# Kernel tuning notes

Measured on AMD Instinct MI355X. Metric: run time of the kernel, lower is better.

The kernel has to match this reference:

```python
import jax, jax.numpy as jnp
import numpy as np
from jax import lax

VOCAB = 256
H = 1024
L = 2
B = 64
T = 512
RESIDUAL = True


def setup_inputs() -> dict:
    key = jax.random.key(0)
    ks = jax.random.split(key, 8)
    s_ih = 1.0 / np.sqrt(H)
    return {
        "X": jax.random.randint(ks[0], (B, T), 0, VOCAB),
        "embed": jax.random.normal(ks[1], (VOCAB, H), dtype=jnp.float32) * 0.02,
        "Wih": jax.random.normal(ks[2], (L, 4 * H, H), dtype=jnp.float32) * s_ih,
        "Whh": jax.random.normal(ks[3], (L, 4 * H, H), dtype=jnp.float32) * s_ih,
        "bih": jax.random.normal(ks[4], (L, 4 * H), dtype=jnp.float32) * s_ih,
        "bhh": jax.random.normal(ks[5], (L, 4 * H), dtype=jnp.float32) * s_ih,
        "Wout": jax.random.normal(ks[6], (VOCAB, H), dtype=jnp.float32) * s_ih,
        "bout": jax.random.normal(ks[7], (VOCAB,), dtype=jnp.float32) * s_ih,
    }


def reference(X, embed, Wih, Whh, bih, bhh, Wout, bout):
    # X: [B, T] int tokens. Original loops over t in [0, T-2]: feeds X[:, t]
    # through an L-layer (residual) LSTM one char at a time, accumulates
    # mean-over-batch cross entropy vs X[:, t+1], then divides by T.
    Bsz, Tlen = X.shape
    n_layers = Wih.shape[0]
    xs = embed[X[:, :-1]]          # [B, T-1, H] embedded inputs
    xs_t = jnp.swapaxes(xs, 0, 1)  # [T-1, B, H] time-major for scan

    def cell(carry, x_t):
        h, c = carry  # each [L, B, H]
        inp = x_t
        hs, cs = [], []
        for l in range(n_layers):
            # torch LSTM gate order: input, forget, cell(g), output
            gates = inp @ Wih[l].T + h[l] @ Whh[l].T + (bih[l] + bhh[l])
            i_g, f_g, g_g, o_g = jnp.split(gates, 4, axis=-1)
            c_l = jax.nn.sigmoid(f_g) * c[l] + jax.nn.sigmoid(i_g) * jnp.tanh(g_g)
            h_l = jax.nn.sigmoid(o_g) * jnp.tanh(c_l)
            hs.append(h_l)
            cs.append(c_l)
            inp = h_l + inp if RESIDUAL else h_l
        return (jnp.stack(hs), jnp.stack(cs)), inp

    init = (jnp.zeros((n_layers, Bsz, xs.shape[-1]), xs.dtype),
            jnp.zeros((n_layers, Bsz, xs.shape[-1]), xs.dtype))
    _, outs = lax.scan(cell, init, xs_t)       # [T-1, B, H]

    logits = outs @ Wout.T + bout              # [T-1, B, V]
    targets = X[:, 1:].T                        # [T-1, B]
    logp = jax.nn.log_softmax(logits, axis=-1)
    ce = -jnp.take_along_axis(logp, targets[..., None], axis=-1)[..., 0]  # [T-1, B]
    loss = ce.mean(axis=1).sum() / Tlen
    return loss
```

## Files before the change

### kernel.cpp

```cpp
#include <hip/hip_runtime.h>
#include <hip/hip_bf16.h>

typedef __hip_bfloat16 bf16;
typedef short v8s __attribute__((ext_vector_type(8)));
typedef float v4f __attribute__((ext_vector_type(4)));
typedef float v16f __attribute__((ext_vector_type(16)));
typedef unsigned long long u64;

static __device__ __forceinline__ float bf2f(bf16 x) { return __bfloat162float(x); }
static __device__ __forceinline__ unsigned short bfbits(float f) {
    bf16 t = __float2bfloat16(f);
    return *(unsigned short*)&t;
}
static __device__ __forceinline__ float fast_tanh(float x) {
    float e = __expf(-2.f * x);
    return (1.f - e) / (1.f + e);
}

__global__ __launch_bounds__(256) void k_zero(float* __restrict__ zbase, float* __restrict__ loss) {
    int idx = blockIdx.x * 256 + threadIdx.x;
    if (idx < 140288) zbase[idx] = 0.0f;
    if (idx == 0) loss[0] = 0.0f;
}

__global__ __launch_bounds__(256) void k_convert_w(const float* __restrict__ Wih,
                                                   const float* __restrict__ Whh,
                                                   bf16* __restrict__ Wb) {
    int idx = blockIdx.x * 256 + threadIdx.x;
    int k2 = idx & 2047;
    int ln = idx >> 11;
    float v = (k2 < 1024) ? Wih[ln * 1024 + k2] : Whh[ln * 1024 + (k2 - 1024)];
    Wb[idx] = __float2bfloat16(v);
}

__global__ __launch_bounds__(256) void k_convert_small(const float* __restrict__ Wout,
                                                       const float* __restrict__ bih,
                                                       const float* __restrict__ bhh,
                                                       bf16* __restrict__ Wob,
                                                       float* __restrict__ bsum) {
    int idx = blockIdx.x * 256 + threadIdx.x;
    if (idx < 262144) Wob[idx] = __float2bfloat16(Wout[idx]);
    int bidx = idx - 262144;
    if (bidx >= 0 && bidx < 8192) bsum[bidx] = bih[bidx] + bhh[bidx];
}

__global__ __launch_bounds__(256) void k_embed(const int* __restrict__ X,
                                               const float* __restrict__ embed,
                                               bf16* __restrict__ x0) {
    int bi = blockIdx.x;
    int kc = bi & 3;
    int tb = bi >> 2;
    int b  = tb & 63;
    int t  = tb >> 6;
    int k  = kc * 256 + threadIdx.x;
    int tok = X[b * 512 + t];
    x0[(long)tb * 1024 + k] = __float2bfloat16(embed[tok * 1024 + k]);
}

#define GLDI_C(dst, p, o) asm volatile("global_load_dwordx4 %0, %1, off offset:%2"         : "=v"(dst) : "v"(p), "i"(o))
#define GLDI_B(dst, p, o) asm volatile("global_load_dwordx4 %0, %1, off offset:%2 sc0 sc1" : "=v"(dst) : "v"(p), "i"(o))
#define MFMA(acc, a, w) asm volatile("v_mfma_f32_32x32x16_bf16 %0, %1, %2, %0" : "+v"(acc) : "v"(a), "a"(w))
#define VW(n)  asm volatile("s_waitcnt vmcnt(%0)" :: "i"(n))
#define VW0()  asm volatile("s_waitcnt vmcnt(0)")
#define ZACC(a) do { _Pragma("unroll") for (int r_ = 0; r_ < 16; ++r_) a[r_] = 0.f; } while(0)

#define ISSUE(GLD, c, B) do { \
    GLD(B[0], pA0, (c)*128 +  0); GLD(B[1], pA1, (c)*128 +  0); \
    GLD(B[2], pA0, (c)*128 + 32); GLD(B[3], pA1, (c)*128 + 32); \
    GLD(B[4], pA0, (c)*128 + 64); GLD(B[5], pA1, (c)*128 + 64); \
    GLD(B[6], pA0, (c)*128 + 96); GLD(B[7], pA1, (c)*128 + 96); } while(0)

#define CHUNK(c, B) do { _Pragma("unroll") for (int i_ = 0; i_ < 4; ++i_) { \
    MFMA(acc00, B[2*i_],   wa0[(c)*4+i_]); \
    MFMA(acc10, B[2*i_+1], wa0[(c)*4+i_]); \
    MFMA(acc01, B[2*i_],   wa1[(c)*4+i_]); \
    MFMA(acc11, B[2*i_+1], wa1[(c)*4+i_]); } } while(0)

#define PIPE(GLD) do { \
    ISSUE(GLD,0,bufa); ISSUE(GLD,1,bufb); ISSUE(GLD,2,bufc); ISSUE(GLD,3,bufd); \
    VW(24); CHUNK(0,bufa); ISSUE(GLD,4,bufa); \
    VW(24); CHUNK(1,bufb); ISSUE(GLD,5,bufb); \
    VW(24); CHUNK(2,bufc); ISSUE(GLD,6,bufc); \
    VW(24); CHUNK(3,bufd); ISSUE(GLD,7,bufd); \
    VW(24); CHUNK(4,bufa); \
    VW(16); CHUNK(5,bufb); \
    VW(8);  CHUNK(6,bufc); \
    VW(0);  CHUNK(7,bufd); } while(0)

#define WRGP(OP) do { _Pragma("unroll") for (int r_ = 0; r_ < 16; ++r_) { \
    const int grow_ = (r_&3) + ((r_>>2)<<3) + ((l>>5)<<2); \
    gp[q&1][grow_][l&31]          OP acc00[r_]; \
    gp[q&1][grow_][32+(l&31)]     OP acc01[r_]; \
    gp[q&1][32+grow_][l&31]       OP acc10[r_]; \
    gp[q&1][32+grow_][32+(l&31)]  OP acc11[r_]; } } while(0)

__global__ __launch_bounds__(256, 1) void k_lstm(bf16* __restrict__ x0all,
                                                 bf16* __restrict__ x1buf,
                                                 bf16* __restrict__ h0buf,
                                                 bf16* __restrict__ h1buf,
                                                 const bf16* __restrict__ Wb,
                                                 const float* __restrict__ bsum,
                                                 unsigned* bar) {
    __shared__ float gp[2][64][67];
    __shared__ float c_lds[64][17];
    __shared__ float b_lds[64];

    const int g     = blockIdx.x;
    const int layer = g >> 6;
    const int j     = g & 63;
    const int tid   = threadIdx.x;
    const int l     = tid & 63;
    const int q     = tid >> 6;

    unsigned* cnt = bar;

    if (tid < 64) b_lds[tid] = bsum[layer * 4096 + (tid >> 4) * 1024 + (j << 4) + (tid & 15)];
    for (int i = tid; i < 64 * 17; i += 256) ((float*)c_lds)[i] = 0.f;

    const int nl0 = l & 31, nl1 = 32 + (l & 31);
    const long N0 = (long)((nl0 >> 4) * 1024 + (j << 4) + (nl0 & 15));
    const long N1 = (long)((nl1 >> 4) * 1024 + (j << 4) + (nl1 & 15));
    const bf16* wp0 = Wb + (long)layer * 8388608 + N0 * 2048 + q * 512 + ((l >> 5) << 3);
    const bf16* wp1 = Wb + (long)layer * 8388608 + N1 * 2048 + q * 512 + ((l >> 5) << 3);
    v8s wa0[32], wa1[32];
#pragma unroll
    for (int kk = 0; kk < 32; ++kk) {
        wa0[kk] = *(const v8s*)(wp0 + kk * 16);
        asm volatile("" : "+a"(wa0[kk]));
        wa1[kk] = *(const v8s*)(wp1 + kk * 16);
        asm volatile("" : "+a"(wa1[kk]));
    }

    const int ab = tid >> 2;
    const int dq = tid & 3;
    const bool prewave = (layer == 0) && (q < 2);

#pragma unroll 1
    for (int s = 0; s < 512; ++s) {
        const bool act = (layer == 0) ? (s < 511) : (s >= 1);
        const bf16* xop = x0all + (long)s * 65536;
        const bf16* x1p = x1buf + ((s + 1) & 1) * 65536;
        const bf16* h0p = h0buf + ((s + 1) & 1) * 65536;
        const bf16* h1p = h1buf + ((s + 1) & 1) * 65536;
        bf16* hdst  = (layer ? h1buf : h0buf) + (s & 1) * 65536;
        bf16* x1dst = x1buf + (s & 1) * 65536;
        bf16* res1  = x0all + (long)(s - 1) * 65536;

        const bf16* base = (layer == 0) ? ((q < 2) ? xop : h0p)
                                        : ((q < 2) ? x1p : h1p);
        const bf16* pA0 = base + ((q & 1) << 9) + (l & 31) * 1024 + ((l >> 5) << 3);
        const bf16* pA1 = pA0 + 32 * 1024;

        v16f acc00, acc01, acc10, acc11;
        v8s bufa[8], bufb[8], bufc[8], bufd[8];

        if (act && prewave) {
            ZACC(acc00); ZACC(acc01); ZACC(acc10); ZACC(acc11);
            PIPE(GLDI_C);
            WRGP(=);
        }
        if (tid == 0 && s > 0) {
            const unsigned tgt = 128u * (unsigned)s;
            while (__hip_atomic_load(cnt, __ATOMIC_RELAXED, __HIP_MEMORY_SCOPE_AGENT) < tgt) {}
        }
        __syncthreads();
        if (act && !prewave) {
            ZACC(acc00); ZACC(acc01); ZACC(acc10); ZACC(acc11);
            PIPE(GLDI_B);
            if (q < 2) WRGP(=);
        }
        __syncthreads();
        if (act && q >= 2) WRGP(+=);
        __syncthreads();

        if (act) {
            u64 xv;
            if (layer == 0) {
                xv = *(const u64*)(xop + ab * 1024 + (j << 4) + dq * 4);
            } else {
                const bf16* xrp = x1p + ab * 1024 + (j << 4) + dq * 4;
                asm volatile("global_load_dwordx2 %0, %1, off sc0 sc1" : "=v"(xv) : "v"(xrp));
            }
            float hv4[4];
#pragma unroll
            for (int i = 0; i < 4; ++i) {
                const int d = dq * 4 + i;
                const float gi = gp[0][ab][d]      + gp[1][ab][d]      + b_lds[d];
                const float gf = gp[0][ab][16 + d] + gp[1][ab][16 + d] + b_lds[16 + d];
                const float gg = gp[0][ab][32 + d] + gp[1][ab][32 + d] + b_lds[32 + d];
                const float go = gp[0][ab][48 + d] + gp[1][ab][48 + d] + b_lds[48 + d];
                const float si = 1.f / (1.f + __expf(-gi));
                const float sf = 1.f / (1.f + __expf(-gf));
                const float so = 1.f / (1.f + __expf(-go));
                const float tg = fast_tanh(gg);
                const float cn = sf * c_lds[ab][d] + si * tg;
                c_lds[ab][d] = cn;
                hv4[i] = so * fast_tanh(cn);
            }
            if (layer != 0) VW0();
            u64 hv64 = 0, rv64 = 0;
#pragma unroll
            for (int i = 0; i < 4; ++i) {
                const unsigned us = (unsigned)((xv >> (16 * i)) & 0xffffu);
                const float rv = hv4[i] + __uint_as_float(us << 16);
                hv64 |= (u64)bfbits(hv4[i]) << (16 * i);
                rv64 |= (u64)bfbits(rv) << (16 * i);
            }
            const int off = ab * 1024 + (j << 4) + dq * 4;
            bf16* hp = hdst + off;
            asm volatile("global_store_dwordx2 %0, %1, off sc0 sc1" :: "v"(hp), "v"(hv64) : "memory");
            if (layer == 0) {
                bf16* rp = x1dst + off;
                asm volatile("global_store_dwordx2 %0, %1, off sc0 sc1" :: "v"(rp), "v"(rv64) : "memory");
            } else {
                *(u64*)(res1 + off) = rv64;
            }
        }
        VW0();
        __syncthreads();
        if (tid == 0)
            __hip_atomic_fetch_add(cnt, 1u, __ATOMIC_RELAXED, __HIP_MEMORY_SCOPE_AGENT);
    }
}

__global__ __launch_bounds__(256) void k_final(const bf16* __restrict__ outAll,
                                               const bf16* __restrict__ Wob,
                                               const float* __restrict__ bout,
                                               const int* __restrict__ X,
                                               float* __restrict__ loss) {
    const int t    = blockIdx.x;
    const int tid  = threadIdx.x;
    const int lane = tid & 63;
    const int w    = tid >> 6;
    const int col  = lane & 15;
    const int oct  = lane >> 4;
    const bf16* arow = outAll + ((long)t * 64 + (w << 4) + col) * 1024 + (oct << 3);
    v4f acc[16];
#pragma unroll
    for (int nt = 0; nt < 16; ++nt) acc[nt] = (v4f){0.f, 0.f, 0.f, 0.f};
    for (int k0 = 0; k0 < 1024; k0 += 32) {
        v8s a = *(const v8s*)(arow + k0);
#pragma unroll
        for (int nt = 0; nt < 16; ++nt) {
            v8s bb = *(const v8s*)(Wob + ((nt << 4) + col) * 1024 + (oct << 3) + k0);
            acc[nt] = __builtin_amdgcn_mfma_f32_16x16x32_bf16(a, bb, acc[nt], 0, 0, 0);
        }
    }
#pragma unroll
    for (int nt = 0; nt < 16; ++nt) {
        const float bb = bout[(nt << 4) + col];
        acc[nt][0] += bb; acc[nt][1] += bb; acc[nt][2] += bb; acc[nt][3] += bb;
    }
    float ce_sum = 0.f;
#pragma unroll
    for (int r = 0; r < 4; ++r) {
        float mx = -3.4e38f;
#pragma unroll
        for (int nt = 0; nt < 16; ++nt) mx = fmaxf(mx, acc[nt][r]);
#pragma unroll
        for (int mm = 1; mm < 16; mm <<= 1) mx = fmaxf(mx, __shfl_xor(mx, mm, 64));
        float ss = 0.f;
#pragma unroll
        for (int nt = 0; nt < 16; ++nt) ss += __expf(acc[nt][r] - mx);
#pragma unroll
        for (int mm = 1; mm < 16; mm <<= 1) ss += __shfl_xor(ss, mm, 64);
        const int b   = (w << 4) + (oct << 2) + r;
        const int tok = X[b * 512 + t + 1];
        float lt = 0.f;
#pragma unroll
        for (int nt = 0; nt < 16; ++nt)
            if ((tok >> 4) == nt) lt = acc[nt][r];
        if ((tok & 15) == col)
            ce_sum += mx + __logf(ss) - lt;
    }
#pragma unroll
    for (int mm = 1; mm < 64; mm <<= 1) ce_sum += __shfl_xor(ce_sum, mm, 64);
    if (lane == 0) atomicAdd(loss, ce_sum * (1.0f / 32768.0f));
}

extern "C" void kernel_launch(void* const* d_in, const int* in_sizes, int n_in,
                              void* d_out, int out_size, void* d_ws, size_t ws_size,
                              hipStream_t stream) {
    const int*   X     = (const int*)  d_in[0];
    const float* embed = (const float*)d_in[1];
    const float* Wih   = (const float*)d_in[2];
    const float* Whh   = (const float*)d_in[3];
    const float* bih   = (const float*)d_in[4];
    const float* bhh   = (const float*)d_in[5];
    const float* Wout  = (const float*)d_in[6];
    const float* bout  = (const float*)d_in[7];
    float* loss = (float*)d_out;

    char* ws = (char*)d_ws;
    bf16*     x0all = (bf16*)(ws + 0);
    bf16*     Wb    = (bf16*)(ws + 66977792);
    bf16*     Wob   = (bf16*)(ws + 100532224);
    bf16*     x1buf = (bf16*)(ws + 101056512);
    bf16*     h0buf = (bf16*)(ws + 101318656);
    bf16*     h1buf = (bf16*)(ws + 101580800);
    float*    bsum  = (float*)(ws + 101842944);
    unsigned* bar   = (unsigned*)(ws + 101875712);
    float*    zbase = (float*)(ws + 101318656);

    if (ws_size < 101879808u) return;

    k_zero<<<548, 256, 0, stream>>>(zbase, loss);
    k_convert_w<<<65536, 256, 0, stream>>>(Wih, Whh, Wb);
    k_convert_small<<<1056, 256, 0, stream>>>(Wout, bih, bhh, Wob, bsum);
    k_embed<<<130816, 256, 0, stream>>>(X, embed, x0all);

    void* args[] = {&x0all, &x1buf, &h0buf, &h1buf, &Wb, &bsum, &bar};
    hipLaunchCooperativeKernel((void*)k_lstm, dim3(128), dim3(256), args, 0, stream);

    k_final<<<511, 256, 0, stream>>>(x0all, Wob, bout, X, loss);
}
```

Before: 6.822 ms.

## Split grid barrier counter into per-group cache lines with acquire fence

Replaces the single global arrival counter with 16 counters, one per group of 8 blocks, each on its own cache line. Layer-0 blocks wait only on layer-0 lines, and layer-1 blocks wait on all lines. The spin loop takes the minimum over the lines, sleeps briefly between polls, and issues an agent-scope acquire fence. Activation loads now use ordinary cached loads instead of sc0 sc1 system-coherent loads, relying on the fence for visibility. This aims to cut atomic contention and the cost of coherent loads, at the risk of stale data if the fence does not cover non-coherent L2 paths.

Result: no change. 6.742 ms (-1.2%).

```diff
diff --git a/kernel.cpp b/kernel.cpp
--- a/kernel.cpp
+++ b/kernel.cpp
@@ -57,18 +57,17 @@
     x0[(long)tb * 1024 + k] = __float2bfloat16(embed[tok * 1024 + k]);
 }
 
-#define GLDI_C(dst, p, o) asm volatile("global_load_dwordx4 %0, %1, off offset:%2"         : "=v"(dst) : "v"(p), "i"(o))
-#define GLDI_B(dst, p, o) asm volatile("global_load_dwordx4 %0, %1, off offset:%2 sc0 sc1" : "=v"(dst) : "v"(p), "i"(o))
+#define GLDI(dst, p, o) asm volatile("global_load_dwordx4 %0, %1, off offset:%2" : "=v"(dst) : "v"(p), "i"(o))
 #define MFMA(acc, a, w) asm volatile("v_mfma_f32_32x32x16_bf16 %0, %1, %2, %0" : "+v"(acc) : "v"(a), "a"(w))
 #define VW(n)  asm volatile("s_waitcnt vmcnt(%0)" :: "i"(n))
 #define VW0()  asm volatile("s_waitcnt vmcnt(0)")
 #define ZACC(a) do { _Pragma("unroll") for (int r_ = 0; r_ < 16; ++r_) a[r_] = 0.f; } while(0)
 
-#define ISSUE(GLD, c, B) do { \
-    GLD(B[0], pA0, (c)*128 +  0); GLD(B[1], pA1, (c)*128 +  0); \
-    GLD(B[2], pA0, (c)*128 + 32); GLD(B[3], pA1, (c)*128 + 32); \
-    GLD(B[4], pA0, (c)*128 + 64); GLD(B[5], pA1, (c)*128 + 64); \
-    GLD(B[6], pA0, (c)*128 + 96); GLD(B[7], pA1, (c)*128 + 96); } while(0)
+#define ISSUE(c, B) do { \
+    GLDI(B[0], pA0, (c)*128 +  0); GLDI(B[1], pA1, (c)*128 +  0); \
+    GLDI(B[2], pA0, (c)*128 + 32); GLDI(B[3], pA1, (c)*128 + 32); \
+    GLDI(B[4], pA0, (c)*128 + 64); GLDI(B[5], pA1, (c)*128 + 64); \
+    GLDI(B[6], pA0, (c)*128 + 96); GLDI(B[7], pA1, (c)*128 + 96); } while(0)
 
 #define CHUNK(c, B) do { _Pragma("unroll") for (int i_ = 0; i_ < 4; ++i_) { \
     MFMA(acc00, B[2*i_],   wa0[(c)*4+i_]); \
@@ -76,12 +75,12 @@
     MFMA(acc01, B[2*i_],   wa1[(c)*4+i_]); \
     MFMA(acc11, B[2*i_+1], wa1[(c)*4+i_]); } } while(0)
 
-#define PIPE(GLD) do { \
-    ISSUE(GLD,0,bufa); ISSUE(GLD,1,bufb); ISSUE(GLD,2,bufc); ISSUE(GLD,3,bufd); \
-    VW(24); CHUNK(0,bufa); ISSUE(GLD,4,bufa); \
-    VW(24); CHUNK(1,bufb); ISSUE(GLD,5,bufb); \
-    VW(24); CHUNK(2,bufc); ISSUE(GLD,6,bufc); \
-    VW(24); CHUNK(3,bufd); ISSUE(GLD,7,bufd); \
+#define PIPE() do { \
+    ISSUE(0,bufa); ISSUE(1,bufb); ISSUE(2,bufc); ISSUE(3,bufd); \
+    VW(24); CHUNK(0,bufa); ISSUE(4,bufa); \
+    VW(24); CHUNK(1,bufb); ISSUE(5,bufb); \
+    VW(24); CHUNK(2,bufc); ISSUE(6,bufc); \
+    VW(24); CHUNK(3,bufd); ISSUE(7,bufd); \
     VW(24); CHUNK(4,bufa); \
     VW(16); CHUNK(5,bufb); \
     VW(8);  CHUNK(6,bufc); \
@@ -112,7 +111,7 @@
     const int l     = tid & 63;
     const int q     = tid >> 6;
 
-    unsigned* cnt = bar;
+    unsigned* myline = bar + ((layer << 3) + (j & 7)) * 32;
 
     if (tid < 64) b_lds[tid] = bsum[layer * 4096 + (tid >> 4) * 1024 + (j << 4) + (tid & 15)];
     for (int i = tid; i < 64 * 17; i += 256) ((float*)c_lds)[i] = 0.f;
@@ -134,6 +133,7 @@
     const int ab = tid >> 2;
     const int dq = tid & 3;
     const bool prewave = (layer == 0) && (q < 2);
+    const int nlines = (layer == 0) ? 8 : 16;
 
 #pragma unroll 1
     for (int s = 0; s < 512; ++s) {
@@ -156,17 +156,29 @@
 
         if (act && prewave) {
             ZACC(acc00); ZACC(acc01); ZACC(acc10); ZACC(acc11);
-            PIPE(GLDI_C);
+            PIPE();
             WRGP(=);
         }
         if (tid == 0 && s > 0) {
-            const unsigned tgt = 128u * (unsigned)s;
-            while (__hip_atomic_load(cnt, __ATOMIC_RELAXED, __HIP_MEMORY_SCOPE_AGENT) < tgt) {}
+            const unsigned tgt = 8u * (unsigned)s;
+            for (;;) {
+                unsigned mn = ~0u;
+#pragma unroll
+                for (int i = 0; i < 16; ++i) {
+                    if (i < nlines) {
+                        unsigned v = __hip_atomic_load(bar + i * 32, __ATOMIC_RELAXED, __HIP_MEMORY_SCOPE_AGENT);
+                        mn = (v < mn) ? v : mn;
+                    }
+                }
+                if (mn >= tgt) break;
+                __builtin_amdgcn_s_sleep(1);
+            }
+            __builtin_amdgcn_fence(__ATOMIC_ACQUIRE, "agent");
         }
         __syncthreads();
         if (act && !prewave) {
             ZACC(acc00); ZACC(acc01); ZACC(acc10); ZACC(acc11);
-            PIPE(GLDI_B);
+            PIPE();
             if (q < 2) WRGP(=);
         }
         __syncthreads();
@@ -174,13 +186,9 @@
         __syncthreads();
 
         if (act) {
-            u64 xv;
-            if (layer == 0) {
-                xv = *(const u64*)(xop + ab * 1024 + (j << 4) + dq * 4);
-            } else {
-                const bf16* xrp = x1p + ab * 1024 + (j << 4) + dq * 4;
-                asm volatile("global_load_dwordx2 %0, %1, off sc0 sc1" : "=v"(xv) : "v"(xrp));
-            }
+            const int off = ab * 1024 + (j << 4) + dq * 4;
+            const u64 xv = (layer == 0) ? *(const u64*)(xop + off)
+                                        : *(const u64*)(x1p + off);
             float hv4[4];
 #pragma unroll
             for (int i = 0; i < 4; ++i) {
@@ -197,7 +205,6 @@
                 c_lds[ab][d] = cn;
                 hv4[i] = so * fast_tanh(cn);
             }
-            if (layer != 0) VW0();
             u64 hv64 = 0, rv64 = 0;
 #pragma unroll
             for (int i = 0; i < 4; ++i) {
@@ -206,20 +213,15 @@
                 hv64 |= (u64)bfbits(hv4[i]) << (16 * i);
                 rv64 |= (u64)bfbits(rv) << (16 * i);
             }
-            const int off = ab * 1024 + (j << 4) + dq * 4;
             bf16* hp = hdst + off;
             asm volatile("global_store_dwordx2 %0, %1, off sc0 sc1" :: "v"(hp), "v"(hv64) : "memory");
-            if (layer == 0) {
-                bf16* rp = x1dst + off;
-                asm volatile("global_store_dwordx2 %0, %1, off sc0 sc1" :: "v"(rp), "v"(rv64) : "memory");
-            } else {
-                *(u64*)(res1 + off) = rv64;
-            }
+            bf16* rp = (layer == 0) ? (x1dst + off) : (res1 + off);
+            asm volatile("global_store_dwordx2 %0, %1, off sc0 sc1" :: "v"(rp), "v"(rv64) : "memory");
         }
         VW0();
         __syncthreads();
         if (tid == 0)
-            __hip_atomic_fetch_add(cnt, 1u, __ATOMIC_RELAXED, __HIP_MEMORY_SCOPE_AGENT);
+            __hip_atomic_fetch_add(myline, 1u, __ATOMIC_RELAXED, __HIP_MEMORY_SCOPE_AGENT);
     }
 }
 
```

## Replace single global barrier counter with striped counters and per-XCC leader broadcast

Applied to the files above, without the earlier changes.

Each block now increments one of 16 cache-line-separated counters instead of a single shared atomic counter. One leader block per XCC polls the minimum of all 16 counters, sleeping between polls, then writes a generation value to a per-XCC line. The other blocks spin on that line with an L2-coherent load and fall back to checking the counters themselves every 64 iterations. This is meant to cut atomic contention and cross-XCC polling traffic in the per-timestep grid barrier, at the cost of an extra broadcast hop and a dependence on the extra barrier memory being zeroed. The layer-1 residual store also now uses the same sc0 sc1 store instruction as layer 0.

Result: slower. 10.34 ms (+51.6%).

```diff
diff --git a/kernel.cpp b/kernel.cpp
--- a/kernel.cpp
+++ b/kernel.cpp
@@ -94,6 +94,16 @@
     gp[q&1][32+grow_][l&31]       OP acc10[r_]; \
     gp[q&1][32+grow_][32+(l&31)]  OP acc11[r_]; } } while(0)
 
+static __device__ __forceinline__ unsigned min16(const unsigned* bar) {
+    unsigned mn = ~0u;
+#pragma unroll
+    for (int i = 0; i < 16; ++i) {
+        unsigned v = __hip_atomic_load(bar + i * 32, __ATOMIC_RELAXED, __HIP_MEMORY_SCOPE_AGENT);
+        mn = (v < mn) ? v : mn;
+    }
+    return mn;
+}
+
 __global__ __launch_bounds__(256, 1) void k_lstm(bf16* __restrict__ x0all,
                                                  bf16* __restrict__ x1buf,
                                                  bf16* __restrict__ h0buf,
@@ -112,7 +122,15 @@
     const int l     = tid & 63;
     const int q     = tid >> 6;
 
-    unsigned* cnt = bar;
+    unsigned* myline = bar + ((layer << 3) + (j & 7)) * 32;
+
+    unsigned xcc;
+    asm volatile("s_getreg_b32 %0, hwreg(HW_REG_XCC_ID)" : "=s"(xcc));
+    unsigned* genp = bar + 512 + (xcc & 7) * 32;
+    bool lead = false;
+    if (tid == 0)
+        lead = (__hip_atomic_fetch_add(bar + 768 + (xcc & 7), 1u,
+                                       __ATOMIC_RELAXED, __HIP_MEMORY_SCOPE_AGENT) == 0);
 
     if (tid < 64) b_lds[tid] = bsum[layer * 4096 + (tid >> 4) * 1024 + (j << 4) + (tid & 15)];
     for (int i = tid; i < 64 * 17; i += 256) ((float*)c_lds)[i] = 0.f;
@@ -160,8 +178,21 @@
             WRGP(=);
         }
         if (tid == 0 && s > 0) {
-            const unsigned tgt = 128u * (unsigned)s;
-            while (__hip_atomic_load(cnt, __ATOMIC_RELAXED, __HIP_MEMORY_SCOPE_AGENT) < tgt) {}
+            const unsigned tgt = 8u * (unsigned)s;
+            if (lead) {
+                while (min16(bar) < tgt) __builtin_amdgcn_s_sleep(1);
+                asm volatile("global_store_dword %0, %1, off"
+                             :: "v"(genp), "v"((unsigned)s) : "memory");
+            } else {
+                int k = 0;
+                for (;;) {
+                    unsigned v;
+                    asm volatile("global_load_dword %0, %1, off sc0\n\t"
+                                 "s_waitcnt vmcnt(0)" : "=v"(v) : "v"(genp));
+                    if (v >= (unsigned)s) break;
+                    if ((++k & 63) == 0 && min16(bar) >= tgt) break;
+                }
+            }
         }
         __syncthreads();
         if (act && !prewave) {
@@ -174,11 +205,12 @@
         __syncthreads();
 
         if (act) {
+            const int off = ab * 1024 + (j << 4) + dq * 4;
             u64 xv;
             if (layer == 0) {
-                xv = *(const u64*)(xop + ab * 1024 + (j << 4) + dq * 4);
+                xv = *(const u64*)(xop + off);
             } else {
-                const bf16* xrp = x1p + ab * 1024 + (j << 4) + dq * 4;
+                const bf16* xrp = x1p + off;
                 asm volatile("global_load_dwordx2 %0, %1, off sc0 sc1" : "=v"(xv) : "v"(xrp));
             }
             float hv4[4];
@@ -206,20 +238,15 @@
                 hv64 |= (u64)bfbits(hv4[i]) << (16 * i);
                 rv64 |= (u64)bfbits(rv) << (16 * i);
             }
-            const int off = ab * 1024 + (j << 4) + dq * 4;
             bf16* hp = hdst + off;
             asm volatile("global_store_dwordx2 %0, %1, off sc0 sc1" :: "v"(hp), "v"(hv64) : "memory");
-            if (layer == 0) {
-                bf16* rp = x1dst + off;
-                asm volatile("global_store_dwordx2 %0, %1, off sc0 sc1" :: "v"(rp), "v"(rv64) : "memory");
-            } else {
-                *(u64*)(res1 + off) = rv64;
-            }
+            bf16* rp = (layer == 0) ? (x1dst + off) : (res1 + off);
+            asm volatile("global_store_dwordx2 %0, %1, off sc0 sc1" :: "v"(rp), "v"(rv64) : "memory");
         }
         VW0();
         __syncthreads();
         if (tid == 0)
-            __hip_atomic_fetch_add(cnt, 1u, __ATOMIC_RELAXED, __HIP_MEMORY_SCOPE_AGENT);
+            __hip_atomic_fetch_add(myline, 1u, __ATOMIC_RELAXED, __HIP_MEMORY_SCOPE_AGENT);
     }
 }
 
```

## Split global step barrier into per-line counters polled by a full wave

Applied to the files above, without the earlier changes.

Replaces the single global atomic counter that all 128 blocks incremented and thread 0 spun on with 24 cache-line-separated counters: 8 per layer for step completion, plus 8 read-done lines that layer-1 blocks bump once they have consumed their inputs. A whole wave polls the relevant lines in parallel with a ballot, so there is less contention on one address and a layer-1 block's readers can be tracked separately. The residual/x loads are also hoisted earlier (before the barrier for layer 0, into the GEMM phase for layer 1), and the layer-1 residual store now uses the same cache-bypassing store. The cost is more atomic traffic and a more complex dependency scheme that must correctly cover buffer reuse.

Measured after the change: 6.024 ms. 1.13x faster.

```diff
diff --git a/kernel.cpp b/kernel.cpp
--- a/kernel.cpp
+++ b/kernel.cpp
@@ -112,7 +112,8 @@
     const int l     = tid & 63;
     const int q     = tid >> 6;
 
-    unsigned* cnt = bar;
+    unsigned* myline = bar + ((layer << 3) + (j & 7)) * 32;
+    unsigned* rdline = bar + (16 + (j & 7)) * 32;
 
     if (tid < 64) b_lds[tid] = bsum[layer * 4096 + (tid >> 4) * 1024 + (j << 4) + (tid & 15)];
     for (int i = tid; i < 64 * 17; i += 256) ((float*)c_lds)[i] = 0.f;
@@ -133,7 +134,11 @@
 
     const int ab = tid >> 2;
     const int dq = tid & 3;
+    const int off_ = ab * 1024 + (j << 4) + dq * 4;
     const bool prewave = (layer == 0) && (q < 2);
+    const int li = l & 31;
+    const bool lineused = (layer == 0) ? (li < 8 || (li >= 16 && li < 24))
+                                       : (li < 16);
 
 #pragma unroll 1
     for (int s = 0; s < 512; ++s) {
@@ -153,34 +158,41 @@
 
         v16f acc00, acc01, acc10, acc11;
         v8s bufa[8], bufb[8], bufc[8], bufd[8];
-
+        u64 xv = 0;
+
+        if (act && layer == 0) xv = *(const u64*)(xop + off_);
         if (act && prewave) {
             ZACC(acc00); ZACC(acc01); ZACC(acc10); ZACC(acc11);
             PIPE(GLDI_C);
             WRGP(=);
         }
-        if (tid == 0 && s > 0) {
-            const unsigned tgt = 128u * (unsigned)s;
-            while (__hip_atomic_load(cnt, __ATOMIC_RELAXED, __HIP_MEMORY_SCOPE_AGENT) < tgt) {}
+        if (s > 0 && q == 0) {
+            const unsigned* lp = bar + li * 32;
+            const unsigned req = lineused ? 8u * (unsigned)s : 0u;
+            for (;;) {
+                unsigned v;
+                asm volatile("global_load_dword %0, %1, off sc0 sc1\n\t"
+                             "s_waitcnt vmcnt(0)" : "=v"(v) : "v"(lp));
+                if (__ballot(v >= req) == ~0ull) break;
+            }
         }
         __syncthreads();
         if (act && !prewave) {
+            if (layer == 1) {
+                const bf16* xrp = x1p + off_;
+                asm volatile("global_load_dwordx2 %0, %1, off sc0 sc1" : "=v"(xv) : "v"(xrp));
+            }
             ZACC(acc00); ZACC(acc01); ZACC(acc10); ZACC(acc11);
             PIPE(GLDI_B);
             if (q < 2) WRGP(=);
         }
         __syncthreads();
+        if (layer == 1 && tid == 0)
+            __hip_atomic_fetch_add(rdline, 1u, __ATOMIC_RELAXED, __HIP_MEMORY_SCOPE_AGENT);
         if (act && q >= 2) WRGP(+=);
         __syncthreads();
 
         if (act) {
-            u64 xv;
-            if (layer == 0) {
-                xv = *(const u64*)(xop + ab * 1024 + (j << 4) + dq * 4);
-            } else {
-                const bf16* xrp = x1p + ab * 1024 + (j << 4) + dq * 4;
-                asm volatile("global_load_dwordx2 %0, %1, off sc0 sc1" : "=v"(xv) : "v"(xrp));
-            }
             float hv4[4];
 #pragma unroll
             for (int i = 0; i < 4; ++i) {
@@ -197,7 +209,6 @@
                 c_lds[ab][d] = cn;
                 hv4[i] = so * fast_tanh(cn);
             }
-            if (layer != 0) VW0();
             u64 hv64 = 0, rv64 = 0;
 #pragma unroll
             for (int i = 0; i < 4; ++i) {
@@ -206,20 +217,15 @@
                 hv64 |= (u64)bfbits(hv4[i]) << (16 * i);
                 rv64 |= (u64)bfbits(rv) << (16 * i);
             }
-            const int off = ab * 1024 + (j << 4) + dq * 4;
-            bf16* hp = hdst + off;
+            bf16* hp = hdst + off_;
             asm volatile("global_store_dwordx2 %0, %1, off sc0 sc1" :: "v"(hp), "v"(hv64) : "memory");
-            if (layer == 0) {
-                bf16* rp = x1dst + off;
-                asm volatile("global_store_dwordx2 %0, %1, off sc0 sc1" :: "v"(rp), "v"(rv64) : "memory");
-            } else {
-                *(u64*)(res1 + off) = rv64;
-            }
+            bf16* rp = (layer == 0) ? (x1dst + off_) : (res1 + off_);
+            asm volatile("global_store_dwordx2 %0, %1, off sc0 sc1" :: "v"(rp), "v"(rv64) : "memory");
         }
         VW0();
         __syncthreads();
         if (tid == 0)
-            __hip_atomic_fetch_add(cnt, 1u, __ATOMIC_RELAXED, __HIP_MEMORY_SCOPE_AGENT);
+            __hip_atomic_fetch_add(myline, 1u, __ATOMIC_RELAXED, __HIP_MEMORY_SCOPE_AGENT);
     }
 }
 
```
